# Optimization experiments

Hardware: AMD Instinct MI355X
Metric: run time of the kernel (lower is better)

## Reference

```python
import jax, jax.numpy as jnp
import numpy as np

B, N, E, H = 2, 2048, 1024, 16
D = E // H  # head dim = 64


def setup_inputs() -> dict:
    key = jax.random.key(0)
    ks = jax.random.split(key, 5)
    s = 0.02
    return {
        "x": jax.random.normal(ks[0], (B, N, E), dtype=jnp.float32),
        "w_qkv": jax.random.normal(ks[1], (3 * E, E), dtype=jnp.float32) * s,
        "b_qkv": jax.random.normal(ks[2], (3 * E,), dtype=jnp.float32) * s,
        "w_proj": jax.random.normal(ks[3], (E, E), dtype=jnp.float32) * s,
        "b_proj": jax.random.normal(ks[4], (E,), dtype=jnp.float32) * s,
    }


def reference(x, w_qkv, b_qkv, w_proj, b_proj):
    # qkv projection: [B, N, 3E]
    qkv = x @ w_qkv.T + b_qkv
    # einops 'b n (h d qkv) -> qkv b h n d': qkv index is INNERMOST in the split
    qkv = qkv.reshape(B, N, H, D, 3)
    qkv = jnp.transpose(qkv, (4, 0, 2, 1, 3))  # [3, B, H, N, D]
    q, k, v = qkv[0], qkv[1], qkv[2]
    scale = 1.0 / jnp.sqrt(jnp.asarray(D, dtype=x.dtype))
    att = jnp.einsum('bhnd,bhmd->bhnm', q, k) * scale  # [B, H, N, N]
    att = jax.nn.softmax(att, axis=-1)
    out = jnp.einsum('bhnm,bhmd->bhnd', att, v)  # [B, H, N, D]
    out = jnp.transpose(out, (0, 2, 1, 3)).reshape(B, N, E)  # b n (h d)
    return out @ w_proj.T + b_proj
```

## Files before the change

kernel.cpp:

```cpp
#include <hip/hip_runtime.h>
#include <hip/hip_bf16.h>
#include <math.h>

#define B_   2
#define N_   2048
#define E_   1024
#define H_   16
#define D_   64
#define E3_  3072
#define M_   (B_ * N_)

#define QSCALE 0.18033688011112042f

using short8 = __attribute__((ext_vector_type(8))) short;
using f32x4  = __attribute__((ext_vector_type(4))) float;
using uint2v = __attribute__((ext_vector_type(2))) unsigned int;

#define MFMA16(a, b, c) __builtin_amdgcn_mfma_f32_16x16x32_bf16((a), (b), (c), 0, 0, 0)

__device__ __forceinline__ unsigned short f2bf(float f) {
    __hip_bfloat16 h = __float2bfloat16(f);
    return __builtin_bit_cast(unsigned short, h);
}

__device__ __forceinline__ float fast_exp2(float x) {
#if __has_builtin(__builtin_amdgcn_exp2f)
    return __builtin_amdgcn_exp2f(x);
#else
    return exp2f(x);
#endif
}

__device__ __forceinline__ unsigned int pack_bf16_rh(float lo, float hi) {
    unsigned int ulo = __builtin_bit_cast(unsigned int, lo) + 0x8000u;
    unsigned int uhi = __builtin_bit_cast(unsigned int, hi) + 0x8000u;
#if __has_builtin(__builtin_amdgcn_perm)
    return __builtin_amdgcn_perm(uhi, ulo, 0x07060302u);
#else
    return (uhi & 0xFFFF0000u) | (ulo >> 16);
#endif
}

__device__ __forceinline__ void gl16(const void* g, void* l) {
    __builtin_amdgcn_global_load_lds(
        (__attribute__((address_space(1))) const void*)g,
        (__attribute__((address_space(3))) void*)l, 16, 0, 0);
}

__global__ __launch_bounds__(256) void convert_kernel(
    const float* __restrict__ x, const float* __restrict__ wq,
    const float* __restrict__ wp, const float* __restrict__ b_qkv,
    unsigned short* __restrict__ xb, unsigned short* __restrict__ wqp,
    unsigned short* __restrict__ wpb, float* __restrict__ bias_perm)
{
    if (blockIdx.x == 4096) {
        for (int q = threadIdx.x; q < E3_; q += 256) {
            const int c = q >> 10, rem = q & 1023;
            const int h = rem >> 6, d = rem & 63;
            float v = b_qkv[h * 192 + d * 3 + c];
            if (c == 0) v *= QSCALE;
            bias_perm[q] = v;
        }
        return;
    }
    const int o = (blockIdx.x * 256 + threadIdx.x) * 8;
    const float* src;
    unsigned short* dst;
    if (o < 4194304) {
        src = x + o; dst = xb + o;
    } else if (o < 7340032) {
        const int oo = o - 4194304;
        const int s = oo >> 10, k = oo & 1023;
        const int c = s >> 10, rem = s & 1023;
        const int h = rem >> 6, d = rem & 63;
        src = wq + (size_t)(h * 192 + d * 3 + c) * E_ + k;
        dst = wqp + oo;
    } else {
        const int oo = o - 7340032;
        src = wp + oo; dst = wpb + oo;
    }
    float4 a = *(const float4*)src;
    float4 b = *(const float4*)(src + 4);
    uint2v p0, p1;
    p0.x = pack_bf16_rh(a.x, a.y); p0.y = pack_bf16_rh(a.z, a.w);
    p1.x = pack_bf16_rh(b.x, b.y); p1.y = pack_bf16_rh(b.z, b.w);
    *(uint2v*)dst = p0;
    *(uint2v*)(dst + 4) = p1;
}

#define GEMM_STAGE(Aglob, Bglob)                                             \
    {                                                                        \
        _Pragma("unroll")                                                    \
        for (int i2 = 0; i2 < 2; ++i2) {                                     \
            const int chunk = wv * 128 + i2 * 64 + lane;                     \
            const int row = chunk >> 2;                                      \
            const int gcg = (chunk & 3) ^ ((row >> 1) & 3);                  \
            const int lbase = (wv * 128 + i2 * 64) * 8;                      \
            gl16(Aglob + (size_t)(bm + row) * E_ + k0 + gcg * 8, &As[lbase]);\
            gl16(Bglob + (size_t)(bn + row) * E_ + k0 + gcg * 8, &Bs[lbase]);\
        }                                                                    \
    }

#define GEMM_COMPUTE(MARR, NARR)                                             \
    {                                                                        \
        const int sw = (l15 >> 1) & 3;                                       \
        short8 af[4], bf[4];                                                 \
        _Pragma("unroll")                                                    \
        for (int i = 0; i < 4; ++i) {                                        \
            const int ra = wr * 64 + i * 16 + l15;                           \
            const int rb = wc * 64 + i * 16 + l15;                           \
            af[i] = *(const short8*)&MARR[ra * 32 + ((quad ^ sw) * 8)];      \
            bf[i] = *(const short8*)&NARR[rb * 32 + ((quad ^ sw) * 8)];      \
        }                                                                    \
        _Pragma("unroll")                                                    \
        for (int i = 0; i < 4; ++i)                                          \
            _Pragma("unroll")                                                \
            for (int j = 0; j < 4; ++j)                                      \
                acc[i][j] = MFMA16(af[i], bf[j], acc[i][j]);                 \
    }

#define GEMM_PROLOG                                                          \
    const int t    = threadIdx.x;                                            \
    const int wv   = t >> 6, lane = t & 63;                                  \
    const int quad = lane >> 4, l15 = lane & 15;                             \
    const int wr   = wv & 1, wc = wv >> 1;                                   \
    f32x4 acc[4][4];                                                         \
    _Pragma("unroll")                                                        \
    for (int i = 0; i < 4; ++i)                                              \
        _Pragma("unroll")                                                    \
        for (int j = 0; j < 4; ++j) acc[i][j] = (f32x4){0.f, 0.f, 0.f, 0.f};

__global__ __launch_bounds__(256) void qkv_qk_kernel(
    const unsigned short* __restrict__ A, const unsigned short* __restrict__ Bm,
    const float* __restrict__ bias_perm,
    unsigned short* __restrict__ Q, unsigned short* __restrict__ K)
{
    __shared__ __attribute__((aligned(16))) unsigned short As[128 * 32];
    __shared__ __attribute__((aligned(16))) unsigned short Bs[128 * 32];
    GEMM_PROLOG
    const int bm = blockIdx.y * 128;
    const int bn = blockIdx.x * 128;

    for (int k0 = 0; k0 < E_; k0 += 32) {
        __syncthreads();
        GEMM_STAGE(A, Bm);
        __syncthreads();
        GEMM_COMPUTE(Bs, As);
    }

    const int c = bn >> 10;
    const float scale = (c == 0) ? QSCALE : 1.0f;
    unsigned short* dst0 = (c == 0) ? Q : K;
#pragma unroll
    for (int i = 0; i < 4; ++i) {
        const int s0 = bn + wr * 64 + i * 16 + quad * 4;
        const int h  = (s0 >> 6) & 15;
        const int d0 = s0 & 63;
        const float4 bq = *(const float4*)(bias_perm + s0);
#pragma unroll
        for (int j = 0; j < 4; ++j) {
            const int row = bm + wc * 64 + j * 16 + l15;
            const int b   = row >> 11, n = row & (N_ - 1);
            const float v0 = fmaf(acc[i][j][0], scale, bq.x);
            const float v1 = fmaf(acc[i][j][1], scale, bq.y);
            const float v2 = fmaf(acc[i][j][2], scale, bq.z);
            const float v3 = fmaf(acc[i][j][3], scale, bq.w);
            uint2v pk;
            pk.x = pack_bf16_rh(v0, v1);
            pk.y = pack_bf16_rh(v2, v3);
            *(uint2v*)(dst0 + (((size_t)b * H_ + h) * N_ + n) * D_ + d0) = pk;
        }
    }
}

__global__ __launch_bounds__(256) void qkv_v_kernel(
    const unsigned short* __restrict__ A, const unsigned short* __restrict__ Bm,
    const float* __restrict__ bias_perm, unsigned short* __restrict__ VT)
{
    __shared__ __attribute__((aligned(16))) unsigned short As[128 * 32];
    __shared__ __attribute__((aligned(16))) unsigned short Bs[128 * 32];
    GEMM_PROLOG
    const int bm = blockIdx.y * 128;
    const int bn = 2048 + blockIdx.x * 128;

    for (int k0 = 0; k0 < E_; k0 += 32) {
        __syncthreads();
        GEMM_STAGE(A, Bm);
        __syncthreads();
        GEMM_COMPUTE(As, Bs);
    }

#pragma unroll
    for (int j = 0; j < 4; ++j) {
        const int s = bn + wc * 64 + j * 16 + l15;
        const int h = (s >> 6) & 15, d = s & 63;
        const float bv = bias_perm[s];
#pragma unroll
        for (int i = 0; i < 4; ++i) {
            const int row0 = bm + wr * 64 + i * 16 + quad * 4;
            const int b    = row0 >> 11, n0 = row0 & (N_ - 1);
            const float v0 = acc[i][j][0] + bv;
            const float v1 = acc[i][j][1] + bv;
            const float v2 = acc[i][j][2] + bv;
            const float v3 = acc[i][j][3] + bv;
            uint2v pk;
            pk.x = pack_bf16_rh(v0, v1);
            pk.y = pack_bf16_rh(v2, v3);
            *(uint2v*)(VT + (((size_t)b * H_ + h) * D_ + d) * N_ + n0) = pk;
        }
    }
}

__global__ __launch_bounds__(256) void attn_kernel(
    const unsigned short* __restrict__ Q, const unsigned short* __restrict__ K,
    const unsigned short* __restrict__ VT, unsigned short* __restrict__ CTX)
{
    __shared__ __attribute__((aligned(16))) unsigned short Ks[64 * 72];
    __shared__ __attribute__((aligned(16))) unsigned short Vs[64 * 72];
    __shared__ __attribute__((aligned(16))) unsigned short Ps[4][16 * 72];

    const int t    = threadIdx.x;
    const int wv   = t >> 6, lane = t & 63;
    const int quad = lane >> 4, l15 = lane & 15;
    const int qt   = blockIdx.x & 31;
    const int bh   = blockIdx.x >> 5;
    const int r0   = t >> 3, c8 = (t & 7) * 8;

    const unsigned short* Kp = K + (size_t)bh * N_ * D_;
    const unsigned short* Vp = VT + (size_t)bh * D_ * N_;
    const unsigned short* Qp = Q + ((size_t)bh * N_ + qt * 64 + wv * 16 + l15) * D_;

    const short8 qf0 = *(const short8*)(Qp + quad * 8);
    const short8 qf1 = *(const short8*)(Qp + 32 + quad * 8);

    f32x4 O[4];
#pragma unroll
    for (int i = 0; i < 4; ++i) O[i] = (f32x4){0.f, 0.f, 0.f, 0.f};
    f32x4 lsum4 = {0.f, 0.f, 0.f, 0.f};

    for (int kt = 0; kt < N_ / 64; ++kt) {
#pragma unroll
        for (int p = 0; p < 2; ++p) {
            const int rr = r0 + p * 32;
            *(short8*)&Ks[rr * 72 + c8] =
                *(const short8*)(Kp + (size_t)(kt * 64 + rr) * D_ + c8);
            *(short8*)&Vs[rr * 72 + c8] =
                *(const short8*)(Vp + (size_t)rr * N_ + kt * 64 + c8);
        }
        __syncthreads();

        f32x4 st[4];
#pragma unroll
        for (int kb = 0; kb < 4; ++kb) st[kb] = (f32x4){0.f, 0.f, 0.f, 0.f};
#pragma unroll
        for (int kb = 0; kb < 4; ++kb) {
            const int krow = (kb * 16 + l15) * 72;
            const short8 kf0 = *(const short8*)&Ks[krow + quad * 8];
            const short8 kf1 = *(const short8*)&Ks[krow + 32 + quad * 8];
            st[kb] = MFMA16(kf0, qf0, st[kb]);
            st[kb] = MFMA16(kf1, qf1, st[kb]);
        }

#pragma unroll
        for (int kb = 0; kb < 4; ++kb) {
            f32x4 pv;
#pragma unroll
            for (int g = 0; g < 4; ++g) pv[g] = fast_exp2(st[kb][g]);
            lsum4 += pv;
            uint2v pk;
            pk.x = pack_bf16_rh(pv[0], pv[1]);
            pk.y = pack_bf16_rh(pv[2], pv[3]);
            *(uint2v*)&Ps[wv][l15 * 72 + kb * 16 + quad * 4] = pk;
        }

#pragma unroll
        for (int ks = 0; ks < 2; ++ks) {
            const short8 pf = *(const short8*)&Ps[wv][l15 * 72 + ks * 32 + quad * 8];
#pragma unroll
            for (int nt = 0; nt < 4; ++nt) {
                const short8 vf =
                    *(const short8*)&Vs[(nt * 16 + l15) * 72 + ks * 32 + quad * 8];
                O[nt] = MFMA16(pf, vf, O[nt]);
            }
        }
        __syncthreads();
    }

    float lt = lsum4[0] + lsum4[1] + lsum4[2] + lsum4[3];
    lt += __shfl_xor(lt, 16, 64);
    lt += __shfl_xor(lt, 32, 64);

    const int b = bh >> 4, h = bh & 15;
#pragma unroll
    for (int g = 0; g < 4; ++g) {
        const float lg  = __shfl(lt, quad * 4 + g, 64);
        const float inv = 1.0f / lg;
        const int qrow  = qt * 64 + wv * 16 + quad * 4 + g;
#pragma unroll
        for (int nt = 0; nt < 4; ++nt)
            CTX[((size_t)b * N_ + qrow) * E_ + h * D_ + nt * 16 + l15] =
                f2bf(O[nt][g] * inv);
    }
}

__global__ __launch_bounds__(256) void proj_kernel(
    const unsigned short* __restrict__ A, const unsigned short* __restrict__ Bm,
    const float* __restrict__ bias, float* __restrict__ out)
{
    __shared__ __attribute__((aligned(16))) unsigned short As[128 * 32];
    __shared__ __attribute__((aligned(16))) unsigned short Bs[128 * 32];
    GEMM_PROLOG
    const int bm = blockIdx.y * 128;
    const int bn = blockIdx.x * 128;

    for (int k0 = 0; k0 < E_; k0 += 32) {
        __syncthreads();
        GEMM_STAGE(A, Bm);
        __syncthreads();
        GEMM_COMPUTE(Bs, As);
    }

#pragma unroll
    for (int i = 0; i < 4; ++i) {
        const int col0 = bn + wr * 64 + i * 16 + quad * 4;
        const float4 bp = *(const float4*)(bias + col0);
#pragma unroll
        for (int j = 0; j < 4; ++j) {
            const int row = bm + wc * 64 + j * 16 + l15;
            float4 o;
            o.x = acc[i][j][0] + bp.x;
            o.y = acc[i][j][1] + bp.y;
            o.z = acc[i][j][2] + bp.z;
            o.w = acc[i][j][3] + bp.w;
            *(float4*)(out + (size_t)row * E_ + col0) = o;
        }
    }
}

extern "C" void kernel_launch(void* const* d_in, const int* in_sizes, int n_in,
                              void* d_out, int out_size, void* d_ws, size_t ws_size,
                              hipStream_t stream)
{
    const float* x      = (const float*)d_in[0];
    const float* w_qkv  = (const float*)d_in[1];
    const float* b_qkv  = (const float*)d_in[2];
    const float* w_proj = (const float*)d_in[3];
    const float* b_proj = (const float*)d_in[4];
    float* out = (float*)d_out;

    unsigned short* xb  = (unsigned short*)d_ws;
    unsigned short* wqp = xb  + 4194304;
    unsigned short* wpb = wqp + 3145728;
    unsigned short* Q   = wpb + 1048576;
    unsigned short* K   = Q   + 4194304;
    unsigned short* VT  = K   + 4194304;
    unsigned short* CTX = VT  + 4194304;
    float* bias_perm    = (float*)(CTX + 4194304);

    dim3 blk(256);
    convert_kernel<<<dim3(4097), blk, 0, stream>>>(
        x, w_qkv, w_proj, b_qkv, xb, wqp, wpb, bias_perm);

    qkv_qk_kernel<<<dim3(16, 32), blk, 0, stream>>>(xb, wqp, bias_perm, Q, K);
    qkv_v_kernel<<<dim3(8, 32), blk, 0, stream>>>(xb, wqp, bias_perm, VT);

    attn_kernel<<<dim3(B_ * H_ * (N_ / 64)), blk, 0, stream>>>(Q, K, VT, CTX);

    proj_kernel<<<dim3(8, 32), blk, 0, stream>>>(CTX, wpb, b_proj, out);
}
```

Baseline: 219.0 us.

## Double-buffer GEMM and attention tiles, merge QKV kernels, enlarge attention query tile

The GEMM kernels switch to double-buffered LDS so the next K-slice is fetched while the current one is computed, which drops one barrier per iteration. The separate QK and V projection kernels become one launch that branches on the column block. The attention kernel now gives each wave 32 query rows and register-prefetches K/V tiles two steps ahead into double-buffered LDS. This is meant to hide global latency and reuse K/V fragments across more queries, at the cost of more LDS and registers per block and half as many attention blocks.

```diff
diff --git a/kernel.cpp b/kernel.cpp
--- a/kernel.cpp
+++ b/kernel.cpp
@@ -88,7 +88,7 @@
     *(uint2v*)(dst + 4) = p1;
 }
 
-#define GEMM_STAGE(Aglob, Bglob)                                             \
+#define GEMM_STAGE(dstA, dstB, Aglob, Bglob, k0)                             \
     {                                                                        \
         _Pragma("unroll")                                                    \
         for (int i2 = 0; i2 < 2; ++i2) {                                     \
@@ -96,8 +96,10 @@
             const int row = chunk >> 2;                                      \
             const int gcg = (chunk & 3) ^ ((row >> 1) & 3);                  \
             const int lbase = (wv * 128 + i2 * 64) * 8;                      \
-            gl16(Aglob + (size_t)(bm + row) * E_ + k0 + gcg * 8, &As[lbase]);\
-            gl16(Bglob + (size_t)(bn + row) * E_ + k0 + gcg * 8, &Bs[lbase]);\
+            gl16(Aglob + (size_t)(bm + row) * E_ + (k0) + gcg * 8,           \
+                 &dstA[lbase]);                                              \
+            gl16(Bglob + (size_t)(bn + row) * E_ + (k0) + gcg * 8,           \
+                 &dstB[lbase]);                                              \
         }                                                                    \
     }
 
@@ -130,83 +132,72 @@
         _Pragma("unroll")                                                    \
         for (int j = 0; j < 4; ++j) acc[i][j] = (f32x4){0.f, 0.f, 0.f, 0.f};
 
-__global__ __launch_bounds__(256) void qkv_qk_kernel(
+__global__ __launch_bounds__(256) void qkv_kernel(
     const unsigned short* __restrict__ A, const unsigned short* __restrict__ Bm,
     const float* __restrict__ bias_perm,
-    unsigned short* __restrict__ Q, unsigned short* __restrict__ K)
+    unsigned short* __restrict__ Q, unsigned short* __restrict__ K,
+    unsigned short* __restrict__ VT)
 {
-    __shared__ __attribute__((aligned(16))) unsigned short As[128 * 32];
-    __shared__ __attribute__((aligned(16))) unsigned short Bs[128 * 32];
+    __shared__ __attribute__((aligned(16))) unsigned short As[2][128 * 32];
+    __shared__ __attribute__((aligned(16))) unsigned short Bs[2][128 * 32];
     GEMM_PROLOG
     const int bm = blockIdx.y * 128;
     const int bn = blockIdx.x * 128;
-
-    for (int k0 = 0; k0 < E_; k0 += 32) {
-        __syncthreads();
-        GEMM_STAGE(A, Bm);
-        __syncthreads();
-        GEMM_COMPUTE(Bs, As);
-    }
-
-    const int c = bn >> 10;
-    const float scale = (c == 0) ? QSCALE : 1.0f;
-    unsigned short* dst0 = (c == 0) ? Q : K;
-#pragma unroll
-    for (int i = 0; i < 4; ++i) {
-        const int s0 = bn + wr * 64 + i * 16 + quad * 4;
-        const int h  = (s0 >> 6) & 15;
-        const int d0 = s0 & 63;
-        const float4 bq = *(const float4*)(bias_perm + s0);
+    const int c  = bn >> 10;
+
+    GEMM_STAGE(As[0], Bs[0], A, Bm, 0);
+    if (c < 2) {
+        for (int it = 0; it < 32; ++it) {
+            const int cur = it & 1;
+            __syncthreads();
+            if (it < 31)
+                GEMM_STAGE(As[cur ^ 1], Bs[cur ^ 1], A, Bm, (it + 1) * 32);
+            GEMM_COMPUTE(Bs[cur], As[cur]);
+        }
+        const float scale = (c == 0) ? QSCALE : 1.0f;
+        unsigned short* dst0 = (c == 0) ? Q : K;
+#pragma unroll
+        for (int i = 0; i < 4; ++i) {
+            const int s0 = bn + wr * 64 + i * 16 + quad * 4;
+            const int h  = (s0 >> 6) & 15;
+            const int d0 = s0 & 63;
+            const float4 bq = *(const float4*)(bias_perm + s0);
+#pragma unroll
+            for (int j = 0; j < 4; ++j) {
+                const int row = bm + wc * 64 + j * 16 + l15;
+                const int b   = row >> 11, n = row & (N_ - 1);
+                const float v0 = fmaf(acc[i][j][0], scale, bq.x);
+                const float v1 = fmaf(acc[i][j][1], scale, bq.y);
+                const float v2 = fmaf(acc[i][j][2], scale, bq.z);
+                const float v3 = fmaf(acc[i][j][3], scale, bq.w);
+                uint2v pk;
+                pk.x = pack_bf16_rh(v0, v1);
+                pk.y = pack_bf16_rh(v2, v3);
+                *(uint2v*)(dst0 + (((size_t)b * H_ + h) * N_ + n) * D_ + d0) = pk;
+            }
+        }
+    } else {
+        for (int it = 0; it < 32; ++it) {
+            const int cur = it & 1;
+            __syncthreads();
+            if (it < 31)
+                GEMM_STAGE(As[cur ^ 1], Bs[cur ^ 1], A, Bm, (it + 1) * 32);
+            GEMM_COMPUTE(As[cur], Bs[cur]);
+        }
 #pragma unroll
         for (int j = 0; j < 4; ++j) {
-            const int row = bm + wc * 64 + j * 16 + l15;
-            const int b   = row >> 11, n = row & (N_ - 1);
-            const float v0 = fmaf(acc[i][j][0], scale, bq.x);
-            const float v1 = fmaf(acc[i][j][1], scale, bq.y);
-            const float v2 = fmaf(acc[i][j][2], scale, bq.z);
-            const float v3 = fmaf(acc[i][j][3], scale, bq.w);
-            uint2v pk;
-            pk.x = pack_bf16_rh(v0, v1);
-            pk.y = pack_bf16_rh(v2, v3);
-            *(uint2v*)(dst0 + (((size_t)b * H_ + h) * N_ + n) * D_ + d0) = pk;
-        }
-    }
-}
-
-__global__ __launch_bounds__(256) void qkv_v_kernel(
-    const unsigned short* __restrict__ A, const unsigned short* __restrict__ Bm,
-    const float* __restrict__ bias_perm, unsigned short* __restrict__ VT)
-{
-    __shared__ __attribute__((aligned(16))) unsigned short As[128 * 32];
-    __shared__ __attribute__((aligned(16))) unsigned short Bs[128 * 32];
-    GEMM_PROLOG
-    const int bm = blockIdx.y * 128;
-    const int bn = 2048 + blockIdx.x * 128;
-
-    for (int k0 = 0; k0 < E_; k0 += 32) {
-        __syncthreads();
-        GEMM_STAGE(A, Bm);
-        __syncthreads();
-        GEMM_COMPUTE(As, Bs);
-    }
-
-#pragma unroll
-    for (int j = 0; j < 4; ++j) {
-        const int s = bn + wc * 64 + j * 16 + l15;
-        const int h = (s >> 6) & 15, d = s & 63;
-        const float bv = bias_perm[s];
-#pragma unroll
-        for (int i = 0; i < 4; ++i) {
-            const int row0 = bm + wr * 64 + i * 16 + quad * 4;
-            const int b    = row0 >> 11, n0 = row0 & (N_ - 1);
-            const float v0 = acc[i][j][0] + bv;
-            const float v1 = acc[i][j][1] + bv;
-            const float v2 = acc[i][j][2] + bv;
-            const float v3 = acc[i][j][3] + bv;
-            uint2v pk;
-            pk.x = pack_bf16_rh(v0, v1);
-            pk.y = pack_bf16_rh(v2, v3);
-            *(uint2v*)(VT + (((size_t)b * H_ + h) * D_ + d) * N_ + n0) = pk;
+            const int s = bn + wc * 64 + j * 16 + l15;
+            const int h = (s >> 6) & 15, d = s & 63;
+            const float bv = bias_perm[s];
+#pragma unroll
+            for (int i = 0; i < 4; ++i) {
+                const int row0 = bm + wr * 64 + i * 16 + quad * 4;
+                const int b    = row0 >> 11, n0 = row0 & (N_ - 1);
+                uint2v pk;
+                pk.x = pack_bf16_rh(acc[i][j][0] + bv, acc[i][j][1] + bv);
+                pk.y = pack_bf16_rh(acc[i][j][2] + bv, acc[i][j][3] + bv);
+                *(uint2v*)(VT + (((size_t)b * H_ + h) * D_ + d) * N_ + n0) = pk;
+            }
         }
     }
 }
@@ -215,91 +206,130 @@
     const unsigned short* __restrict__ Q, const unsigned short* __restrict__ K,
     const unsigned short* __restrict__ VT, unsigned short* __restrict__ CTX)
 {
-    __shared__ __attribute__((aligned(16))) unsigned short Ks[64 * 72];
-    __shared__ __attribute__((aligned(16))) unsigned short Vs[64 * 72];
-    __shared__ __attribute__((aligned(16))) unsigned short Ps[4][16 * 72];
+    __shared__ __attribute__((aligned(16))) unsigned short Ks[2][64 * 72];
+    __shared__ __attribute__((aligned(16))) unsigned short Vs[2][64 * 72];
+    __shared__ __attribute__((aligned(16))) unsigned short Ps[8][16 * 72];
 
     const int t    = threadIdx.x;
     const int wv   = t >> 6, lane = t & 63;
     const int quad = lane >> 4, l15 = lane & 15;
-    const int qt   = blockIdx.x & 31;
-    const int bh   = blockIdx.x >> 5;
+    const int qt   = blockIdx.x & 15;
+    const int bh   = blockIdx.x >> 4;
     const int r0   = t >> 3, c8 = (t & 7) * 8;
 
     const unsigned short* Kp = K + (size_t)bh * N_ * D_;
     const unsigned short* Vp = VT + (size_t)bh * D_ * N_;
-    const unsigned short* Qp = Q + ((size_t)bh * N_ + qt * 64 + wv * 16 + l15) * D_;
-
-    const short8 qf0 = *(const short8*)(Qp + quad * 8);
-    const short8 qf1 = *(const short8*)(Qp + 32 + quad * 8);
-
-    f32x4 O[4];
-#pragma unroll
-    for (int i = 0; i < 4; ++i) O[i] = (f32x4){0.f, 0.f, 0.f, 0.f};
-    f32x4 lsum4 = {0.f, 0.f, 0.f, 0.f};
-
-    for (int kt = 0; kt < N_ / 64; ++kt) {
-#pragma unroll
-        for (int p = 0; p < 2; ++p) {
-            const int rr = r0 + p * 32;
-            *(short8*)&Ks[rr * 72 + c8] =
-                *(const short8*)(Kp + (size_t)(kt * 64 + rr) * D_ + c8);
-            *(short8*)&Vs[rr * 72 + c8] =
-                *(const short8*)(Vp + (size_t)rr * N_ + kt * 64 + c8);
-        }
+
+    short8 qf[2][2];
+#pragma unroll
+    for (int s = 0; s < 2; ++s) {
+        const unsigned short* Qp =
+            Q + ((size_t)bh * N_ + qt * 128 + wv * 32 + s * 16 + l15) * D_;
+        qf[s][0] = *(const short8*)(Qp + quad * 8);
+        qf[s][1] = *(const short8*)(Qp + 32 + quad * 8);
+    }
+
+    f32x4 O[2][4];
+#pragma unroll
+    for (int s = 0; s < 2; ++s)
+#pragma unroll
+        for (int i = 0; i < 4; ++i) O[s][i] = (f32x4){0.f, 0.f, 0.f, 0.f};
+    f32x4 lsum4[2] = {{0.f, 0.f, 0.f, 0.f}, {0.f, 0.f, 0.f, 0.f}};
+
+    short8 kr[2], vr[2];
+#define LOAD_KV(kt)                                                          \
+    {                                                                        \
+        _Pragma("unroll")                                                    \
+        for (int p = 0; p < 2; ++p) {                                        \
+            const int rr = r0 + p * 32;                                      \
+            kr[p] = *(const short8*)(Kp + (size_t)((kt) * 64 + rr) * D_ + c8);\
+            vr[p] = *(const short8*)(Vp + (size_t)rr * N_ + (kt) * 64 + c8); \
+        }                                                                    \
+    }
+#define WRITE_KV(buf)                                                        \
+    {                                                                        \
+        _Pragma("unroll")                                                    \
+        for (int p = 0; p < 2; ++p) {                                        \
+            const int rr = r0 + p * 32;                                      \
+            *(short8*)&Ks[buf][rr * 72 + c8] = kr[p];                        \
+            *(short8*)&Vs[buf][rr * 72 + c8] = vr[p];                        \
+        }                                                                    \
+    }
+
+    LOAD_KV(0);
+    WRITE_KV(0);
+    LOAD_KV(1);
+
+    for (int kt = 0; kt < 32; ++kt) {
+        const int cur = kt & 1;
         __syncthreads();
-
-        f32x4 st[4];
-#pragma unroll
-        for (int kb = 0; kb < 4; ++kb) st[kb] = (f32x4){0.f, 0.f, 0.f, 0.f};
+        if (kt < 31) {
+            WRITE_KV(cur ^ 1);
+            if (kt < 30) LOAD_KV(kt + 2);
+        }
+
+        f32x4 st[2][4];
+#pragma unroll
+        for (int s = 0; s < 2; ++s)
+#pragma unroll
+            for (int kb = 0; kb < 4; ++kb) st[s][kb] = (f32x4){0.f, 0.f, 0.f, 0.f};
 #pragma unroll
         for (int kb = 0; kb < 4; ++kb) {
             const int krow = (kb * 16 + l15) * 72;
-            const short8 kf0 = *(const short8*)&Ks[krow + quad * 8];
-            const short8 kf1 = *(const short8*)&Ks[krow + 32 + quad * 8];
-            st[kb] = MFMA16(kf0, qf0, st[kb]);
-            st[kb] = MFMA16(kf1, qf1, st[kb]);
-        }
-
-#pragma unroll
-        for (int kb = 0; kb < 4; ++kb) {
-            f32x4 pv;
-#pragma unroll
-            for (int g = 0; g < 4; ++g) pv[g] = fast_exp2(st[kb][g]);
-            lsum4 += pv;
-            uint2v pk;
-            pk.x = pack_bf16_rh(pv[0], pv[1]);
-            pk.y = pack_bf16_rh(pv[2], pv[3]);
-            *(uint2v*)&Ps[wv][l15 * 72 + kb * 16 + quad * 4] = pk;
-        }
+            const short8 kf0 = *(const short8*)&Ks[cur][krow + quad * 8];
+            const short8 kf1 = *(const short8*)&Ks[cur][krow + 32 + quad * 8];
+#pragma unroll
+            for (int s = 0; s < 2; ++s) {
+                st[s][kb] = MFMA16(kf0, qf[s][0], st[s][kb]);
+                st[s][kb] = MFMA16(kf1, qf[s][1], st[s][kb]);
+            }
+        }
+
+#pragma unroll
+        for (int s = 0; s < 2; ++s)
+#pragma unroll
+            for (int kb = 0; kb < 4; ++kb) {
+                f32x4 pv;
+#pragma unroll
+                for (int g = 0; g < 4; ++g) pv[g] = fast_exp2(st[s][kb][g]);
+                lsum4[s] += pv;
+                uint2v pk;
+                pk.x = pack_bf16_rh(pv[0], pv[1]);
+                pk.y = pack_bf16_rh(pv[2], pv[3]);
+                *(uint2v*)&Ps[wv * 2 + s][l15 * 72 + kb * 16 + quad * 4] = pk;
+            }
 
 #pragma unroll
         for (int ks = 0; ks < 2; ++ks) {
-            const short8 pf = *(const short8*)&Ps[wv][l15 * 72 + ks * 32 + quad * 8];
+            short8 pf[2];
+            pf[0] = *(const short8*)&Ps[wv * 2 + 0][l15 * 72 + ks * 32 + quad * 8];
+            pf[1] = *(const short8*)&Ps[wv * 2 + 1][l15 * 72 + ks * 32 + quad * 8];
 #pragma unroll
             for (int nt = 0; nt < 4; ++nt) {
                 const short8 vf =
-                    *(const short8*)&Vs[(nt * 16 + l15) * 72 + ks * 32 + quad * 8];
-                O[nt] = MFMA16(pf, vf, O[nt]);
+                    *(const short8*)&Vs[cur][(nt * 16 + l15) * 72 + ks * 32 + quad * 8];
+                O[0][nt] = MFMA16(pf[0], vf, O[0][nt]);
+                O[1][nt] = MFMA16(pf[1], vf, O[1][nt]);
             }
         }
-        __syncthreads();
-    }
-
-    float lt = lsum4[0] + lsum4[1] + lsum4[2] + lsum4[3];
-    lt += __shfl_xor(lt, 16, 64);
-    lt += __shfl_xor(lt, 32, 64);
+    }
 
     const int b = bh >> 4, h = bh & 15;
 #pragma unroll
-    for (int g = 0; g < 4; ++g) {
-        const float lg  = __shfl(lt, quad * 4 + g, 64);
-        const float inv = 1.0f / lg;
-        const int qrow  = qt * 64 + wv * 16 + quad * 4 + g;
-#pragma unroll
-        for (int nt = 0; nt < 4; ++nt)
-            CTX[((size_t)b * N_ + qrow) * E_ + h * D_ + nt * 16 + l15] =
-                f2bf(O[nt][g] * inv);
+    for (int s = 0; s < 2; ++s) {
+        float lt = lsum4[s][0] + lsum4[s][1] + lsum4[s][2] + lsum4[s][3];
+        lt += __shfl_xor(lt, 16, 64);
+        lt += __shfl_xor(lt, 32, 64);
+#pragma unroll
+        for (int g = 0; g < 4; ++g) {
+            const float lg  = __shfl(lt, quad * 4 + g, 64);
+            const float inv = 1.0f / lg;
+            const int qrow  = qt * 128 + wv * 32 + s * 16 + quad * 4 + g;
+#pragma unroll
+            for (int nt = 0; nt < 4; ++nt)
+                CTX[((size_t)b * N_ + qrow) * E_ + h * D_ + nt * 16 + l15] =
+                    f2bf(O[s][nt][g] * inv);
+        }
     }
 }
 
@@ -307,17 +337,19 @@
     const unsigned short* __restrict__ A, const unsigned short* __restrict__ Bm,
     const float* __restrict__ bias, float* __restrict__ out)
 {
-    __shared__ __attribute__((aligned(16))) unsigned short As[128 * 32];
-    __shared__ __attribute__((aligned(16))) unsigned short Bs[128 * 32];
+    __shared__ __attribute__((aligned(16))) unsigned short As[2][128 * 32];
+    __shared__ __attribute__((aligned(16))) unsigned short Bs[2][128 * 32];
     GEMM_PROLOG
     const int bm = blockIdx.y * 128;
     const int bn = blockIdx.x * 128;
 
-    for (int k0 = 0; k0 < E_; k0 += 32) {
+    GEMM_STAGE(As[0], Bs[0], A, Bm, 0);
+    for (int it = 0; it < 32; ++it) {
+        const int cur = it & 1;
         __syncthreads();
-        GEMM_STAGE(A, Bm);
-        __syncthreads();
-        GEMM_COMPUTE(Bs, As);
+        if (it < 31)
+            GEMM_STAGE(As[cur ^ 1], Bs[cur ^ 1], A, Bm, (it + 1) * 32);
+        GEMM_COMPUTE(Bs[cur], As[cur]);
     }
 
 #pragma unroll
@@ -361,10 +393,9 @@
     convert_kernel<<<dim3(4097), blk, 0, stream>>>(
         x, w_qkv, w_proj, b_qkv, xb, wqp, wpb, bias_perm);
 
-    qkv_qk_kernel<<<dim3(16, 32), blk, 0, stream>>>(xb, wqp, bias_perm, Q, K);
-    qkv_v_kernel<<<dim3(8, 32), blk, 0, stream>>>(xb, wqp, bias_perm, VT);
-
-    attn_kernel<<<dim3(B_ * H_ * (N_ / 64)), blk, 0, stream>>>(Q, K, VT, CTX);
+    qkv_kernel<<<dim3(24, 32), blk, 0, stream>>>(xb, wqp, bias_perm, Q, K, VT);
+
+    attn_kernel<<<dim3(B_ * H_ * (N_ / 128)), blk, 0, stream>>>(Q, K, VT, CTX);
 
     proj_kernel<<<dim3(8, 32), blk, 0, stream>>>(CTX, wpb, b_proj, out);
 }
```

Result: faster. 212.3 us (-3.0%).
